# Optimization experiments

Measured on AMD Instinct MI355X. Metric: run time of the kernel, lower is better.

The kernel has to match this reference:

```python
import jax, jax.numpy as jnp
import numpy as np

N_NODES = 40000
N_EDGES = 640000
D = 128


def setup_inputs() -> dict:
    key = jax.random.key(0)
    ks = jax.random.split(key, 7)
    x = jax.random.normal(ks[0], (N_NODES, D), dtype=jnp.float32)
    edge_index = jax.random.randint(ks[1], (2, N_EDGES), 0, N_NODES, dtype=jnp.int64)
    # uniform in [0.5, 1.5) to avoid division blow-up near zero
    edge_attr = jax.random.uniform(ks[2], (N_EDGES,), dtype=jnp.float32) + 0.5
    s = 1.0 / np.sqrt(D)
    W1 = jax.random.uniform(ks[3], (D, D), dtype=jnp.float32, minval=-s, maxval=s)
    b1 = jax.random.uniform(ks[4], (D,), dtype=jnp.float32, minval=-s, maxval=s)
    W2 = jax.random.uniform(ks[5], (D, D), dtype=jnp.float32, minval=-s, maxval=s)
    b2 = jax.random.uniform(ks[6], (D,), dtype=jnp.float32, minval=-s, maxval=s)
    return {"x": x, "edge_index": edge_index, "edge_attr": edge_attr,
            "W1": W1, "b1": b1, "W2": W2, "b2": b2}


def _layer(x, src, dst, edge_attr, W, b, num_nodes):
    # message: gather source features, divide by per-edge scalar
    msg = x[src] / edge_attr[:, None]                      # [E, D]
    # aggregate: scatter-add into destination nodes
    agg = jax.ops.segment_sum(msg, dst, num_segments=num_nodes)  # [N, D]
    # linear (torch: y = x @ W.T + b) then leaky_relu(0.01)
    y = agg @ W.T + b
    return jnp.where(y >= 0, y, 0.01 * y)


def reference(x, edge_index, edge_attr, W1, b1, W2, b2):
    src, dst = edge_index[0], edge_index[1]
    n = x.shape[0]
    x = jnp.maximum(_layer(x, src, dst, edge_attr, W1, b1, n), 0.0)
    x = jnp.maximum(_layer(x, src, dst, edge_attr, W2, b2, n), 0.0)
    return x
```

## Files before the change

### kernel.cpp

```cpp
#include <hip/hip_runtime.h>

#define D 128
#define CAP 64
typedef unsigned short u16;
typedef unsigned int   u32;

typedef __attribute__((ext_vector_type(8))) short short8;
typedef __attribute__((ext_vector_type(4))) float f32x4;

__device__ __forceinline__ u32 f2bf(float f) {
    u32 u = __float_as_uint(f);
    u += 0x7fffu + ((u >> 16) & 1u);
    return u >> 16;
}
__device__ __forceinline__ float2 bf2x2(u32 u) {
    float2 r;
    r.x = __uint_as_float(u << 16);
    r.y = __uint_as_float(u & 0xffff0000u);
    return r;
}

__global__ __launch_bounds__(256) void prep_kernel(
    const float4* __restrict__ x, uint2* __restrict__ xb,
    const float4* __restrict__ W1, const float4* __restrict__ W2,
    uint2* __restrict__ wb1, uint2* __restrict__ wb2,
    const int* __restrict__ src, const int* __restrict__ dst,
    const float* __restrict__ attr, int* __restrict__ counts,
    u32* __restrict__ combo, int E, int n4, int cvtb, int Nper, int N)
{
    const int bid = blockIdx.x;
    const int t   = threadIdx.x;

    if (bid < cvtb) {
        int i = bid * 256 + t;
        if (i < n4) {
            float4 v = x[i];
            uint2 o;
            o.x = f2bf(v.x) | (f2bf(v.y) << 16);
            o.y = f2bf(v.z) | (f2bf(v.w) << 16);
            xb[i] = o;
        }
    } else if (bid < cvtb + 32) {
        int i = (bid - cvtb) * 256 + t;
        const float4* in = (i < 4096) ? W1 : W2;
        uint2* out = (i < 4096) ? wb1 : wb2;
        int k = i & 4095;
        float4 v = in[k];
        uint2 o;
        o.x = f2bf(v.x) | (f2bf(v.y) << 16);
        o.y = f2bf(v.z) | (f2bf(v.w) << 16);
        out[k] = o;
    } else {
        const int sb    = bid - cvtb - 32;
        const int xcd   = sb & 7;
        const int chunk = sb >> 3;
        const int lo    = xcd * Nper;
        const int hi    = min(lo + Nper, N);
        long long e0 = (long long)chunk * 1024 + t * 4;

        if (e0 + 3 < E) {
            int4   s4 = *(const int4*)(src + e0);
            int4   d4 = *(const int4*)(dst + e0);
            float4 a4 = *(const float4*)(attr + e0);
            #pragma unroll
            for (int q = 0; q < 4; ++q) {
                int d = (q == 0) ? d4.x : (q == 1) ? d4.y : (q == 2) ? d4.z : d4.w;
                if (d >= lo && d < hi) {
                    int s = (q == 0) ? s4.x : (q == 1) ? s4.y : (q == 2) ? s4.z : s4.w;
                    float a = (q == 0) ? a4.x : (q == 1) ? a4.y : (q == 2) ? a4.z : a4.w;
                    int r = atomicAdd(&counts[d], 1);
                    if (r < CAP)
                        combo[((long long)d << 6) + r] =
                            (u32)s | (f2bf(1.0f / a) << 16);
                }
            }
        } else {
            for (int q = 0; q < 4; ++q) {
                long long e = e0 + q;
                if (e < E) {
                    int d = dst[e];
                    if (d >= lo && d < hi) {
                        int r = atomicAdd(&counts[d], 1);
                        if (r < CAP)
                            combo[((long long)d << 6) + r] =
                                (u32)src[e] | (f2bf(1.0f / attr[e]) << 16);
                    }
                }
            }
        }
    }
}

template <bool OUT_BF16>
__global__ __launch_bounds__(512) void fused_layer_kernel(
    const u16* __restrict__ X, const u32* __restrict__ combo,
    const int* __restrict__ counts, const u16* __restrict__ Wb,
    const float* __restrict__ bias, void* __restrict__ Yv, int Nper, int N)
{
    __shared__ u16 As[32 * D];

    const int w    = threadIdx.x >> 6;
    const int lane = threadIdx.x & 63;
    const int g    = lane >> 4;
    const int c16  = lane & 15;

    const int xcd   = blockIdx.x & 7;
    const int slice = blockIdx.x >> 3;
    const int nl0   = slice * 32 + w * 4;
    const int nbase = xcd * Nper;

    int cnt4[4]; u32 ce4[4];
    #pragma unroll
    for (int i = 0; i < 4; ++i) {
        int nl = nl0 + i;
        bool v = (nl < Nper) && (nbase + nl < N);
        cnt4[i] = v ? min(counts[nbase + nl], CAP) : 0;
        ce4[i]  = v ? combo[((long long)(nbase + nl) << 6) + lane] : 0u;
    }

    float acc[4][8];
    #pragma unroll
    for (int i = 0; i < 4; ++i)
        #pragma unroll
        for (int c = 0; c < 8; ++c) acc[i][c] = 0.f;

    const int jmax = max(max(cnt4[0], cnt4[1]), max(cnt4[2], cnt4[3]));

    for (int j = 0; j < jmax; j += 4) {
        u32 row[4]; float f[4];
        #pragma unroll
        for (int i = 0; i < 4; ++i) {
            u32 ei = __shfl(ce4[i], j + g);
            bool act = (j + g) < cnt4[i];
            row[i] = act ? (ei & 0xffffu) : 0u;
            f[i]   = act ? __uint_as_float(ei & 0xffff0000u) : 0.f;
        }
        uint4 r[4];
        #pragma unroll
        for (int i = 0; i < 4; ++i)
            r[i] = *(const uint4*)(X + (long long)row[i] * D + c16 * 8);
        #pragma unroll
        for (int i = 0; i < 4; ++i) {
            float2 v;
            v = bf2x2(r[i].x); acc[i][0] += v.x * f[i]; acc[i][1] += v.y * f[i];
            v = bf2x2(r[i].y); acc[i][2] += v.x * f[i]; acc[i][3] += v.y * f[i];
            v = bf2x2(r[i].z); acc[i][4] += v.x * f[i]; acc[i][5] += v.y * f[i];
            v = bf2x2(r[i].w); acc[i][6] += v.x * f[i]; acc[i][7] += v.y * f[i];
        }
    }

    #pragma unroll
    for (int i = 0; i < 4; ++i) {
        #pragma unroll
        for (int c = 0; c < 8; ++c) {
            acc[i][c] += __shfl_xor(acc[i][c], 16);
            acc[i][c] += __shfl_xor(acc[i][c], 32);
        }
        if (g == 0) {
            uint4 o;
            o.x = f2bf(acc[i][0]) | (f2bf(acc[i][1]) << 16);
            o.y = f2bf(acc[i][2]) | (f2bf(acc[i][3]) << 16);
            o.z = f2bf(acc[i][4]) | (f2bf(acc[i][5]) << 16);
            o.w = f2bf(acc[i][6]) | (f2bf(acc[i][7]) << 16);
            int rowi = w * 4 + i;
            int slot = c16 ^ (rowi & 7);
            *(uint4*)&As[rowi * D + slot * 8] = o;
        }
    }

    __syncthreads();

    const int mrow = lane & 15;
    const int kq   = lane >> 4;
    const int h    = w >> 2;
    const int q    = w & 3;
    const int lr0  = h * 16;

    short8 afr[4];
    const u16* asrc = As + (lr0 + mrow) * D;
    #pragma unroll
    for (int ks = 0; ks < 4; ++ks)
        afr[ks] = *(const short8*)(asrc + ((kq + ks * 4) ^ (mrow & 7)) * 8);

    #pragma unroll
    for (int jn = 0; jn < 2; ++jn) {
        const int n0 = q * 32 + jn * 16;
        float bv = bias[n0 + mrow];
        f32x4 acc2 = {bv, bv, bv, bv};
        const u16* wrow = Wb + (long long)(n0 + mrow) * D + kq * 8;
        #pragma unroll
        for (int ks = 0; ks < 4; ++ks) {
            short8 bfr = *(const short8*)(wrow + ks * 32);
            acc2 = __builtin_amdgcn_mfma_f32_16x16x32_bf16(afr[ks], bfr, acc2, 0, 0, 0);
        }
        #pragma unroll
        for (int r = 0; r < 4; ++r) {
            float v = acc2[r] > 0.f ? acc2[r] : 0.f;
            int lrow = lr0 + kq * 4 + r;
            int nl   = slice * 32 + lrow;
            if (nl < Nper && nbase + nl < N) {
                long long off = (long long)(nbase + nl) * D + n0 + mrow;
                if (OUT_BF16)
                    *((u16*)Yv + off) = (u16)f2bf(v);
                else
                    *((float*)Yv + off) = v;
            }
        }
    }
}

extern "C" void kernel_launch(void* const* d_in, const int* in_sizes, int n_in,
                              void* d_out, int out_size, void* d_ws, size_t ws_size,
                              hipStream_t stream)
{
    const float* x    = (const float*)d_in[0];
    const int*   eidx = (const int*)d_in[1];
    const float* attr = (const float*)d_in[2];
    const float* W1   = (const float*)d_in[3];
    const float* b1   = (const float*)d_in[4];
    const float* W2   = (const float*)d_in[5];
    const float* b2   = (const float*)d_in[6];

    const int N = in_sizes[0] / D;
    const int E = in_sizes[2];
    const int* src = eidx;
    const int* dst = eidx + E;
    const int Nper = (N + 7) / 8;

    char* p = (char*)d_ws;
    u16*  xb    = (u16*)p;   p += ((size_t)N * D * 2 + 15) & ~15ULL;
    u16*  aggB  = (u16*)p;   p += ((size_t)N * D * 2 + 15) & ~15ULL;
    u32*  combo = (u32*)p;   p += (size_t)N * CAP * 4;
    u16*  wb1   = (u16*)p;   p += (size_t)D * D * 2;
    u16*  wb2   = (u16*)p;   p += (size_t)D * D * 2;
    int*  counts= (int*)p;

    const int n4    = N * D / 4;
    const int cvtb  = (n4 + 255) / 256;
    const int hfb   = 8 * ((E + 1023) / 1024);
    const int prepb = cvtb + 32 + hfb;
    const int fusedb = 8 * ((Nper + 31) / 32);

    hipMemsetAsync(counts, 0, (size_t)N * 4, stream);
    prep_kernel<<<prepb, 256, 0, stream>>>(
        (const float4*)x, (uint2*)xb, (const float4*)W1, (const float4*)W2,
        (uint2*)wb1, (uint2*)wb2, src, dst, attr, counts,
        combo, E, n4, cvtb, Nper, N);

    fused_layer_kernel<true><<<fusedb, 512, 0, stream>>>(
        xb, combo, counts, wb1, b1, aggB, Nper, N);
    fused_layer_kernel<false><<<fusedb, 512, 0, stream>>>(
        aggB, combo, counts, wb2, b2, d_out, Nper, N);
}
```

Baseline: 199.3 us.

## Bucket each node's incoming edges by source-node XCD partition, halve nodes per block

Each destination node's edge list is split into 8 buckets of 16 slots, keyed by which XCD partition the source node falls in and rotated relative to the destination's XCD. Gathers can then walk the partitions in a fixed order so concurrent blocks hit similar regions of X, which is meant to improve L2 locality. The fused kernel now handles 16 nodes per block (2 per wave) with one MFMA n-tile per wave, doubling the grid. In exchange there are 8x more counters to clear and atomically bump, the edge buffer doubles in size, more divergent short loops run per bucket, and a 16-entry per-bucket cap can drop edges on skewed degree distributions.

```diff
diff --git a/kernel.cpp b/kernel.cpp
--- a/kernel.cpp
+++ b/kernel.cpp
@@ -1,7 +1,7 @@
 #include <hip/hip_runtime.h>
 
 #define D 128
-#define CAP 64
+#define CAPB 16
 typedef unsigned short u16;
 typedef unsigned int   u32;
 
@@ -25,8 +25,8 @@
     const float4* __restrict__ W1, const float4* __restrict__ W2,
     uint2* __restrict__ wb1, uint2* __restrict__ wb2,
     const int* __restrict__ src, const int* __restrict__ dst,
-    const float* __restrict__ attr, int* __restrict__ counts,
-    u32* __restrict__ combo, int E, int n4, int cvtb, int Nper, int N)
+    const float* __restrict__ attr, int* __restrict__ counts2,
+    u32* __restrict__ combo2, int E, int n4, int cvtb, int Nper, int N)
 {
     const int bid = blockIdx.x;
     const int t   = threadIdx.x;
@@ -68,9 +68,10 @@
                 if (d >= lo && d < hi) {
                     int s = (q == 0) ? s4.x : (q == 1) ? s4.y : (q == 2) ? s4.z : s4.w;
                     float a = (q == 0) ? a4.x : (q == 1) ? a4.y : (q == 2) ? a4.z : a4.w;
-                    int r = atomicAdd(&counts[d], 1);
-                    if (r < CAP)
-                        combo[((long long)d << 6) + r] =
+                    int P = ((int)((u32)s / (u32)Nper) + 8 - xcd) & 7;
+                    int r = atomicAdd(&counts2[(d << 3) + P], 1);
+                    if (r < CAPB)
+                        combo2[((long long)d << 7) + (P << 4) + r] =
                             (u32)s | (f2bf(1.0f / a) << 16);
                 }
             }
@@ -80,10 +81,12 @@
                 if (e < E) {
                     int d = dst[e];
                     if (d >= lo && d < hi) {
-                        int r = atomicAdd(&counts[d], 1);
-                        if (r < CAP)
-                            combo[((long long)d << 6) + r] =
-                                (u32)src[e] | (f2bf(1.0f / attr[e]) << 16);
+                        int s = src[e];
+                        int P = ((int)((u32)s / (u32)Nper) + 8 - xcd) & 7;
+                        int r = atomicAdd(&counts2[(d << 3) + P], 1);
+                        if (r < CAPB)
+                            combo2[((long long)d << 7) + (P << 4) + r] =
+                                (u32)s | (f2bf(1.0f / attr[e]) << 16);
                     }
                 }
             }
@@ -93,11 +96,11 @@
 
 template <bool OUT_BF16>
 __global__ __launch_bounds__(512) void fused_layer_kernel(
-    const u16* __restrict__ X, const u32* __restrict__ combo,
-    const int* __restrict__ counts, const u16* __restrict__ Wb,
+    const u16* __restrict__ X, const u32* __restrict__ combo2,
+    const int* __restrict__ counts2, const u16* __restrict__ Wb,
     const float* __restrict__ bias, void* __restrict__ Yv, int Nper, int N)
 {
-    __shared__ u16 As[32 * D];
+    __shared__ u16 As[16 * D];
 
     const int w    = threadIdx.x >> 6;
     const int lane = threadIdx.x & 63;
@@ -106,51 +109,56 @@
 
     const int xcd   = blockIdx.x & 7;
     const int slice = blockIdx.x >> 3;
-    const int nl0   = slice * 32 + w * 4;
+    const int nl0   = slice * 16 + w * 2;
     const int nbase = xcd * Nper;
 
-    int cnt4[4]; u32 ce4[4];
-    #pragma unroll
-    for (int i = 0; i < 4; ++i) {
+    int cntv = 0;
+    if (lane < 16) {
+        int nl = nl0 + (lane >> 3);
+        if (nl < Nper && nbase + nl < N)
+            cntv = counts2[((nbase + nl) << 3) + (lane & 7)];
+    }
+
+    u32 ce_lo[2], ce_hi[2];
+    #pragma unroll
+    for (int i = 0; i < 2; ++i) {
         int nl = nl0 + i;
         bool v = (nl < Nper) && (nbase + nl < N);
-        cnt4[i] = v ? min(counts[nbase + nl], CAP) : 0;
-        ce4[i]  = v ? combo[((long long)(nbase + nl) << 6) + lane] : 0u;
-    }
-
-    float acc[4][8];
-    #pragma unroll
-    for (int i = 0; i < 4; ++i)
+        long long base = (long long)(nbase + nl) << 7;
+        ce_lo[i] = v ? combo2[base + lane]      : 0u;
+        ce_hi[i] = v ? combo2[base + 64 + lane] : 0u;
+    }
+
+    float acc[2][8];
+    #pragma unroll
+    for (int i = 0; i < 2; ++i)
         #pragma unroll
         for (int c = 0; c < 8; ++c) acc[i][c] = 0.f;
 
-    const int jmax = max(max(cnt4[0], cnt4[1]), max(cnt4[2], cnt4[3]));
-
-    for (int j = 0; j < jmax; j += 4) {
-        u32 row[4]; float f[4];
+    #pragma unroll
+    for (int b = 0; b < 8; ++b) {
         #pragma unroll
-        for (int i = 0; i < 4; ++i) {
-            u32 ei = __shfl(ce4[i], j + g);
-            bool act = (j + g) < cnt4[i];
-            row[i] = act ? (ei & 0xffffu) : 0u;
-            f[i]   = act ? __uint_as_float(ei & 0xffff0000u) : 0.f;
-        }
-        uint4 r[4];
-        #pragma unroll
-        for (int i = 0; i < 4; ++i)
-            r[i] = *(const uint4*)(X + (long long)row[i] * D + c16 * 8);
-        #pragma unroll
-        for (int i = 0; i < 4; ++i) {
-            float2 v;
-            v = bf2x2(r[i].x); acc[i][0] += v.x * f[i]; acc[i][1] += v.y * f[i];
-            v = bf2x2(r[i].y); acc[i][2] += v.x * f[i]; acc[i][3] += v.y * f[i];
-            v = bf2x2(r[i].z); acc[i][4] += v.x * f[i]; acc[i][5] += v.y * f[i];
-            v = bf2x2(r[i].w); acc[i][6] += v.x * f[i]; acc[i][7] += v.y * f[i];
-        }
-    }
-
-    #pragma unroll
-    for (int i = 0; i < 4; ++i) {
+        for (int i = 0; i < 2; ++i) {
+            const int cnt = min(__shfl(cntv, i * 8 + b), CAPB);
+            const u32 ces = (b < 4) ? ce_lo[i] : ce_hi[i];
+            const int s0  = (b & 3) << 4;
+            for (int j = 0; j < cnt; j += 4) {
+                u32 e = __shfl(ces, s0 + j + g);
+                bool act = (j + g) < cnt;
+                u32 row = act ? (e & 0xffffu) : 0u;
+                float f = act ? __uint_as_float(e & 0xffff0000u) : 0.f;
+                uint4 r0 = *(const uint4*)(X + (long long)row * D + c16 * 8);
+                float2 v;
+                v = bf2x2(r0.x); acc[i][0] += v.x * f; acc[i][1] += v.y * f;
+                v = bf2x2(r0.y); acc[i][2] += v.x * f; acc[i][3] += v.y * f;
+                v = bf2x2(r0.z); acc[i][4] += v.x * f; acc[i][5] += v.y * f;
+                v = bf2x2(r0.w); acc[i][6] += v.x * f; acc[i][7] += v.y * f;
+            }
+        }
+    }
+
+    #pragma unroll
+    for (int i = 0; i < 2; ++i) {
         #pragma unroll
         for (int c = 0; c < 8; ++c) {
             acc[i][c] += __shfl_xor(acc[i][c], 16);
@@ -162,7 +170,7 @@
             o.y = f2bf(acc[i][2]) | (f2bf(acc[i][3]) << 16);
             o.z = f2bf(acc[i][4]) | (f2bf(acc[i][5]) << 16);
             o.w = f2bf(acc[i][6]) | (f2bf(acc[i][7]) << 16);
-            int rowi = w * 4 + i;
+            int rowi = w * 2 + i;
             int slot = c16 ^ (rowi & 7);
             *(uint4*)&As[rowi * D + slot * 8] = o;
         }
@@ -172,39 +180,33 @@
 
     const int mrow = lane & 15;
     const int kq   = lane >> 4;
-    const int h    = w >> 2;
-    const int q    = w & 3;
-    const int lr0  = h * 16;
 
     short8 afr[4];
-    const u16* asrc = As + (lr0 + mrow) * D;
+    const u16* asrc = As + mrow * D;
     #pragma unroll
     for (int ks = 0; ks < 4; ++ks)
         afr[ks] = *(const short8*)(asrc + ((kq + ks * 4) ^ (mrow & 7)) * 8);
 
-    #pragma unroll
-    for (int jn = 0; jn < 2; ++jn) {
-        const int n0 = q * 32 + jn * 16;
-        float bv = bias[n0 + mrow];
-        f32x4 acc2 = {bv, bv, bv, bv};
-        const u16* wrow = Wb + (long long)(n0 + mrow) * D + kq * 8;
-        #pragma unroll
-        for (int ks = 0; ks < 4; ++ks) {
-            short8 bfr = *(const short8*)(wrow + ks * 32);
-            acc2 = __builtin_amdgcn_mfma_f32_16x16x32_bf16(afr[ks], bfr, acc2, 0, 0, 0);
-        }
-        #pragma unroll
-        for (int r = 0; r < 4; ++r) {
-            float v = acc2[r] > 0.f ? acc2[r] : 0.f;
-            int lrow = lr0 + kq * 4 + r;
-            int nl   = slice * 32 + lrow;
-            if (nl < Nper && nbase + nl < N) {
-                long long off = (long long)(nbase + nl) * D + n0 + mrow;
-                if (OUT_BF16)
-                    *((u16*)Yv + off) = (u16)f2bf(v);
-                else
-                    *((float*)Yv + off) = v;
-            }
+    const int n0 = w * 16;
+    float bv = bias[n0 + mrow];
+    f32x4 acc2 = {bv, bv, bv, bv};
+    const u16* wrow = Wb + (long long)(n0 + mrow) * D + kq * 8;
+    #pragma unroll
+    for (int ks = 0; ks < 4; ++ks) {
+        short8 bfr = *(const short8*)(wrow + ks * 32);
+        acc2 = __builtin_amdgcn_mfma_f32_16x16x32_bf16(afr[ks], bfr, acc2, 0, 0, 0);
+    }
+    #pragma unroll
+    for (int r = 0; r < 4; ++r) {
+        float v = acc2[r] > 0.f ? acc2[r] : 0.f;
+        int lrow = kq * 4 + r;
+        int nl   = slice * 16 + lrow;
+        if (nl < Nper && nbase + nl < N) {
+            long long off = (long long)(nbase + nl) * D + n0 + mrow;
+            if (OUT_BF16)
+                *((u16*)Yv + off) = (u16)f2bf(v);
+            else
+                *((float*)Yv + off) = v;
         }
     }
 }
@@ -228,27 +230,27 @@
     const int Nper = (N + 7) / 8;
 
     char* p = (char*)d_ws;
-    u16*  xb    = (u16*)p;   p += ((size_t)N * D * 2 + 15) & ~15ULL;
-    u16*  aggB  = (u16*)p;   p += ((size_t)N * D * 2 + 15) & ~15ULL;
-    u32*  combo = (u32*)p;   p += (size_t)N * CAP * 4;
-    u16*  wb1   = (u16*)p;   p += (size_t)D * D * 2;
-    u16*  wb2   = (u16*)p;   p += (size_t)D * D * 2;
-    int*  counts= (int*)p;
+    u16*  xb     = (u16*)p;  p += ((size_t)N * D * 2 + 15) & ~15ULL;
+    u16*  aggB   = (u16*)p;  p += ((size_t)N * D * 2 + 15) & ~15ULL;
+    u32*  combo2 = (u32*)p;  p += (size_t)N * 128 * 4;
+    u16*  wb1    = (u16*)p;  p += (size_t)D * D * 2;
+    u16*  wb2    = (u16*)p;  p += (size_t)D * D * 2;
+    int*  counts2= (int*)p;
 
     const int n4    = N * D / 4;
     const int cvtb  = (n4 + 255) / 256;
     const int hfb   = 8 * ((E + 1023) / 1024);
     const int prepb = cvtb + 32 + hfb;
-    const int fusedb = 8 * ((Nper + 31) / 32);
-
-    hipMemsetAsync(counts, 0, (size_t)N * 4, stream);
+    const int fusedb = 8 * ((Nper + 15) / 16);
+
+    hipMemsetAsync(counts2, 0, (size_t)N * 8 * 4, stream);
     prep_kernel<<<prepb, 256, 0, stream>>>(
         (const float4*)x, (uint2*)xb, (const float4*)W1, (const float4*)W2,
-        (uint2*)wb1, (uint2*)wb2, src, dst, attr, counts,
-        combo, E, n4, cvtb, Nper, N);
+        (uint2*)wb1, (uint2*)wb2, src, dst, attr, counts2,
+        combo2, E, n4, cvtb, Nper, N);
 
     fused_layer_kernel<true><<<fusedb, 512, 0, stream>>>(
-        xb, combo, counts, wb1, b1, aggB, Nper, N);
+        xb, combo2, counts2, wb1, b1, aggB, Nper, N);
     fused_layer_kernel<false><<<fusedb, 512, 0, stream>>>(
-        aggB, combo, counts, wb2, b2, d_out, Nper, N);
-}
+        aggB, combo2, counts2, wb2, b2, d_out, Nper, N);
+}
```

Result: no change. 197.0 us (-1.2%).
